# Optimization experiments

Measured on AMD Instinct MI355X. Metric: run time of the kernel, lower is better.

## Reference

```python
import jax, jax.numpy as jnp
import numpy as np
import math

N_LAYERS = 2
N_HEADS = 8
D_MODEL = 512
D_FF = 2048
B = 2
L = 2048
GELU_C = 0.7978845608028654  # sqrt(2/pi)
LN_EPS = 1e-5


def gelu_tanh(x):
    # faithful to the module's custom GELU: 0.5*x*(1+tanh(sqrt(2/pi)*(x+0.044715*x^3)))
    return 0.5 * x * (1.0 + jnp.tanh(GELU_C * (x + 0.044715 * x * x * x)))


def layernorm(x, g, b):
    m = jnp.mean(x, axis=-1, keepdims=True)
    v = jnp.mean((x - m) ** 2, axis=-1, keepdims=True)
    return (x - m) * jax.lax.rsqrt(v + LN_EPS) * g + b


def setup_inputs() -> dict:
    key = jax.random.key(0)
    ks = jax.random.split(key, 24)
    w = lambda k, shape: jax.random.normal(k, shape, dtype=jnp.float32) * 0.02
    inp = {
        "x": jax.random.normal(ks[0], (B, L, D_MODEL), dtype=jnp.float32),
        # tau is exp(tau_learner(...)) in the full model -> positive scalar per batch
        "tau": jax.random.uniform(ks[1], (B, 1), dtype=jnp.float32) + 0.5,
        "delta": jax.random.normal(ks[2], (B, L), dtype=jnp.float32) * 0.1,
        # NStransformer builds an upper-triangular causal mask (True = masked)
        "att_mask": jnp.triu(jnp.ones((L, L), dtype=bool), k=1),
        "Wq": w(ks[3], (N_LAYERS, D_MODEL, D_MODEL)), "bq": jnp.zeros((N_LAYERS, D_MODEL), jnp.float32),
        "Wk": w(ks[4], (N_LAYERS, D_MODEL, D_MODEL)), "bk": jnp.zeros((N_LAYERS, D_MODEL), jnp.float32),
        "Wv": w(ks[5], (N_LAYERS, D_MODEL, D_MODEL)), "bv": jnp.zeros((N_LAYERS, D_MODEL), jnp.float32),
        "Wo": w(ks[6], (N_LAYERS, D_MODEL, D_MODEL)), "bo": jnp.zeros((N_LAYERS, D_MODEL), jnp.float32),
        # conv1/conv2 are kernel_size=1 Conv1d == pointwise linears
        "W1": w(ks[7], (N_LAYERS, D_MODEL, D_FF)), "b1": jnp.zeros((N_LAYERS, D_FF), jnp.float32),
        "W2": w(ks[8], (N_LAYERS, D_FF, D_MODEL)), "b2": jnp.zeros((N_LAYERS, D_MODEL), jnp.float32),
        "ln1_g": jnp.ones((N_LAYERS, D_MODEL), jnp.float32), "ln1_b": jnp.zeros((N_LAYERS, D_MODEL), jnp.float32),
        "ln2_g": jnp.ones((N_LAYERS, D_MODEL), jnp.float32), "ln2_b": jnp.zeros((N_LAYERS, D_MODEL), jnp.float32),
        "lnf_g": jnp.ones((D_MODEL,), jnp.float32), "lnf_b": jnp.zeros((D_MODEL,), jnp.float32),
    }
    return inp


def reference(x, tau, delta, att_mask, Wq, bq, Wk, bk, Wv, bv, Wo, bo,
              W1, b1, W2, b2, ln1_g, ln1_b, ln2_g, ln2_b, lnf_g, lnf_b):
    Bsz, Ls, D = x.shape
    H = N_HEADS
    E = D // H
    scale = 1.0 / math.sqrt(E)
    t = tau[:, None, None, :]    # (B,1) -> (B,1,1,1)
    d = delta[:, None, None, :]  # (B,L) -> (B,1,1,L)
    neg_inf = jnp.float32(-jnp.inf)
    for l in range(N_LAYERS):
        q = (x @ Wq[l] + bq[l]).reshape(Bsz, Ls, H, E)
        k = (x @ Wk[l] + bk[l]).reshape(Bsz, Ls, H, E)
        v = (x @ Wv[l] + bv[l]).reshape(Bsz, Ls, H, E)
        # de-stationary scores: QK^T * tau + delta, then masked softmax
        scores = jnp.einsum('blhe,bshe->bhls', q, k) * t + d  # (B,H,L,S)
        scores = jnp.where(att_mask, neg_inf, scores)
        A = jax.nn.softmax(scale * scores, axis=-1)  # dropout is identity in eval
        V = jnp.einsum('bhls,bshd->blhd', A, v).reshape(Bsz, Ls, D)
        x = (V @ Wo[l] + bo[l]) + x
        xb = layernorm(x, ln1_g[l], ln1_b[l])
        h = gelu_tanh(xb @ W1[l] + b1[l])   # conv1 (k=1)
        o = h @ W2[l] + b2[l]               # conv2 (k=1)
        x = layernorm(o + xb, ln2_g[l], ln2_b[l])
    return layernorm(x, lnf_g, lnf_b)
```

## Files before the change

### kernel.cpp

```cpp
#include <hip/hip_runtime.h>
#include <stdint.h>

#define DM   512
#define DFF  2048
#define NH   8
#define EH   64
#define SEQ  2048
#define NBAT 2
#define NTOK (NBAT*SEQ)
#define LOG2E 1.44269504088896340736f

typedef __attribute__((ext_vector_type(8))) short  s16x8;
typedef __attribute__((ext_vector_type(8))) __bf16 bf16x8;
typedef __attribute__((ext_vector_type(4))) float  f32x4;

__device__ __forceinline__ short f2bf(float f) {
  union { float f; unsigned int i; } c; c.f = f;
  unsigned int x = c.i;
  x += 0x7fffu + ((x >> 16) & 1u);
  return (short)(x >> 16);
}
__device__ __forceinline__ float bf2f(short u) {
  union { unsigned int i; float f; } c;
  c.i = ((unsigned int)(unsigned short)u) << 16;
  return c.f;
}
__device__ __forceinline__ f32x4 mfma16(bf16x8 a, bf16x8 b, f32x4 c) {
  return __builtin_amdgcn_mfma_f32_16x16x32_bf16(a, b, c, 0, 0, 0);
}
__device__ __forceinline__ void gl_lds16(const short* g, short* l) {
  __builtin_amdgcn_global_load_lds(
      (const __attribute__((address_space(1))) unsigned int*)(const void*)g,
      (__attribute__((address_space(3))) unsigned int*)(void*)l, 16, 0, 0);
}

__global__ __launch_bounds__(256) void fill_code_f32(float* __restrict__ out,
                                                     float code)
{
  out[blockIdx.x * 256 + threadIdx.x] = code;
}

__global__ __launch_bounds__(256) void prep_weights(
    const float* __restrict__ Wq, const float* __restrict__ Wk,
    const float* __restrict__ Wv, const float* __restrict__ Wo,
    const float* __restrict__ W1, const float* __restrict__ W2,
    short* __restrict__ Wqkvt, short* __restrict__ Wot,
    short* __restrict__ W1t,   short* __restrict__ W2t)
{
  int gw   = blockIdx.x * 4 + (threadIdx.x >> 6);
  int lane = threadIdx.x & 63;
  int l = gw / 6144;
  int g = gw % 6144;
  const float* src; short* dst; int K, N, gi;
  if (g < 2048) {
    int w = g >> 9; gi = g & 511; K = 512; N = 512;
    src = (w == 0 ? Wq : w == 1 ? Wk : w == 2 ? Wv : Wo) + l * 262144;
    dst = (w < 3) ? (Wqkvt + l * 786432 + w * 262144) : (Wot + l * 262144);
  } else if (g < 4096) {
    gi = g - 2048; K = 512; N = 2048;
    src = W1 + l * 1048576; dst = W1t + l * 1048576;
  } else {
    gi = g - 4096; K = 2048; N = 512;
    src = W2 + l * 1048576; dst = W2t + l * 1048576;
  }
  int nb = N >> 6;
  int n  = (gi % nb) * 64 + lane;
  int k0 = (gi / nb) * 8;
  s16x8 v;
  #pragma unroll
  for (int i = 0; i < 8; i++) v[i] = f2bf(src[(size_t)(k0 + i) * N + n]);
  *(s16x8*)(dst + (size_t)n * K + k0) = v;
}

__global__ __launch_bounds__(256) void cast_kernel(const float* __restrict__ in,
                                                   float* __restrict__ outf,
                                                   short* __restrict__ outb)
{
  int i = blockIdx.x * 256 + threadIdx.x;
  float v = in[i];
  outf[i] = v;
  outb[i] = f2bf(v);
}

template<int TM>
__global__ __launch_bounds__(256) void gemm_bt(
    const short* __restrict__ A, const short* __restrict__ Bt,
    int M, int N, int K, int mode,
    const float* __restrict__ bq, const float* __restrict__ bk,
    const float* __restrict__ bv,
    short* __restrict__ oq, short* __restrict__ okk, short* __restrict__ ov,
    float* of, const float* rf, const short* __restrict__ rb)
{
  __shared__ short As[TM * 32];
  __shared__ short Bs[128 * 32];
  constexpr int MT = TM / 32;
  const int tid  = threadIdx.x;
  const int lane = tid & 63;
  const int wid  = tid >> 6;
  const int lm   = lane & 15, quad = lane >> 4;
  const int nbn  = N >> 7;
  const int m0   = (blockIdx.x / nbn) * TM;
  const int n0   = (blockIdx.x % nbn) << 7;
  const int wm   = (wid & 1) * (TM / 2), wn = (wid >> 1) * 64;

  f32x4 acc[MT][4];
  #pragma unroll
  for (int i = 0; i < MT; i++)
    #pragma unroll
    for (int j = 0; j < 4; j++) acc[i][j] = (f32x4){0.f, 0.f, 0.f, 0.f};

  const short* Abase = A  + (size_t)m0 * K;
  const short* Bbase = Bt + (size_t)n0 * K;

  for (int k0 = 0; k0 < K; k0 += 32) {
    __syncthreads();
    #pragma unroll
    for (int j = 0; j < TM / 64; j++) {
      int c = j * 256 + wid * 64 + lane;
      gl_lds16(Abase + (size_t)(c >> 2) * K + k0 + (c & 3) * 8,
               &As[(j * 256 + wid * 64) * 8]);
    }
    #pragma unroll
    for (int j = 0; j < 2; j++) {
      int c = j * 256 + wid * 64 + lane;
      gl_lds16(Bbase + (size_t)(c >> 2) * K + k0 + (c & 3) * 8,
               &Bs[(j * 256 + wid * 64) * 8]);
    }
    __syncthreads();
    bf16x8 af[MT], bfr[4];
    #pragma unroll
    for (int t = 0; t < MT; t++)
      af[t] = *(const bf16x8*)&As[(wm + t * 16 + lm) * 32 + quad * 8];
    #pragma unroll
    for (int t = 0; t < 4; t++)
      bfr[t] = *(const bf16x8*)&Bs[(wn + t * 16 + lm) * 32 + quad * 8];
    #pragma unroll
    for (int mt = 0; mt < MT; mt++)
      #pragma unroll
      for (int nt = 0; nt < 4; nt++)
        acc[mt][nt] = mfma16(af[mt], bfr[nt], acc[mt][nt]);
  }

  #pragma unroll
  for (int mt = 0; mt < MT; mt++) {
    int row = m0 + wm + mt * 16 + quad * 4;
    #pragma unroll
    for (int nt = 0; nt < 4; nt++) {
      int col = n0 + wn + nt * 16 + lm;
      f32x4 v = acc[mt][nt];
      if (mode == 0) {
        int which = col >> 9; int d = col & 511;
        int hh = d >> 6; int e = d & 63;
        const float* bias = which == 0 ? bq : which == 1 ? bk : bv;
        float bb = bias[d];
        #pragma unroll
        for (int r = 0; r < 4; r++) {
          int tok = row + r; int bI = tok >> 11, li = tok & 2047;
          float val = v[r] + bb;
          if (which == 0)
            oq [(((size_t)bI * NH + hh) * SEQ + li) * EH + e] = f2bf(val);
          else if (which == 1)
            okk[(((size_t)bI * NH + hh) * SEQ + li) * EH + e] = f2bf(val);
          else
            ov [(((size_t)bI * NH + hh) * EH + e) * SEQ + li] = f2bf(val);
        }
      } else if (mode == 1) {
        float bb = bq[col];
        #pragma unroll
        for (int r = 0; r < 4; r++) {
          size_t idx = (size_t)(row + r) * N + col;
          of[idx] = v[r] + bb + rf[idx];
        }
      } else if (mode == 2) {
        float bb = bq[col];
        #pragma unroll
        for (int r = 0; r < 4; r++) {
          float x = v[r] + bb;
          float u = 0.7978845608f * (x + 0.044715f * x * x * x);
          float t = 1.f - 2.f / (1.f + __expf(2.f * u));
          size_t idx = (size_t)(row + r) * N + col;
          oq[idx] = f2bf(0.5f * x * (1.f + t));
        }
      } else {
        float bb = bq[col];
        #pragma unroll
        for (int r = 0; r < 4; r++) {
          size_t idx = (size_t)(row + r) * N + col;
          of[idx] = v[r] + bb + bf2f(rb[idx]);
        }
      }
    }
  }
}

__global__ __launch_bounds__(256) void attn_v7(
    const short* __restrict__ Q, const short* __restrict__ Kg,
    const short* __restrict__ Vt,
    const float* __restrict__ tau, const float* __restrict__ delta,
    short* __restrict__ opart, float* __restrict__ lpart)
{
  __shared__ short Ks[64 * 72];
  __shared__ short Vs[64 * 72];
  __shared__ short Ps[4][16 * 72];
  const int tid  = threadIdx.x;
  const int lane = tid & 63, wid = tid >> 6;
  const int lm = lane & 15, quad = lane >> 4;
  const int t    = blockIdx.x >> 2;
  const int part = blockIdx.x & 3;
  const int qb = 31 - (t & 31);
  const int h  = (t >> 5) & 7;
  const int b  = t >> 8;
  const int q0 = qb * 64;
  const int qw = q0 + wid * 16;
  const size_t bhq = ((size_t)b * NH + h) * SEQ;
  const short* kbase = Kg + bhq * EH;
  const short* vbase = Vt + ((size_t)b * NH + h) * (size_t)(EH * SEQ);

  const int nblk = qb + 1;
  const int kb0 = (nblk * part) >> 2;
  const int kb1 = (nblk * (part + 1)) >> 2;

  bf16x8 qf0 = *(const bf16x8*)(Q + (bhq + qw + lm) * EH + quad * 8);
  bf16x8 qf1 = *(const bf16x8*)(Q + (bhq + qw + lm) * EH + 32 + quad * 8);

  const float st2 = 0.125f * LOG2E * tau[b];
  f32x4 O[4];
  #pragma unroll
  for (int i = 0; i < 4; i++) O[i] = (f32x4){0.f, 0.f, 0.f, 0.f};
  float lr[4] = {0.f, 0.f, 0.f, 0.f};

  const int c0 = tid, c1 = tid + 256;
  const int r0 = c0 >> 3, ch0 = (c0 & 7) * 8;
  const int r1 = c1 >> 3, ch1 = (c1 & 7) * 8;

  for (int kb = kb0; kb < kb1; kb++) {
    const int s0 = kb << 6;
    s16x8 ka = *(const s16x8*)(kbase + (size_t)(s0 + r0) * EH + ch0);
    s16x8 kb_ = *(const s16x8*)(kbase + (size_t)(s0 + r1) * EH + ch1);
    s16x8 va = *(const s16x8*)(vbase + (size_t)r0 * SEQ + s0 + ch0);
    s16x8 vb = *(const s16x8*)(vbase + (size_t)r1 * SEQ + s0 + ch1);
    __syncthreads();
    *(s16x8*)&Ks[r0 * 72 + ch0] = ka;
    *(s16x8*)&Ks[r1 * 72 + ch1] = kb_;
    *(s16x8*)&Vs[r0 * 72 + ch0] = va;
    *(s16x8*)&Vs[r1 * 72 + ch1] = vb;
    __syncthreads();

    f32x4 S[4];
    #pragma unroll
    for (int nt = 0; nt < 4; nt++) {
      S[nt] = (f32x4){0.f, 0.f, 0.f, 0.f};
      S[nt] = mfma16(qf0, *(const bf16x8*)&Ks[(nt*16 + lm) * 72 + quad * 8], S[nt]);
      S[nt] = mfma16(qf1, *(const bf16x8*)&Ks[(nt*16 + lm) * 72 + 32 + quad * 8], S[nt]);
    }
    float dl[4];
    #pragma unroll
    for (int nt = 0; nt < 4; nt++)
      dl[nt] = fmaf(0.125f * LOG2E, delta[(size_t)b * SEQ + s0 + nt * 16 + lm],
                    -8.f);

    const bool diag = (kb == qb);
    #pragma unroll
    for (int r = 0; r < 4; r++) {
      float sc[4];
      #pragma unroll
      for (int nt = 0; nt < 4; nt++) sc[nt] = fmaf(st2, S[nt][r], dl[nt]);
      if (diag) {
        int rowq = qw + quad * 4 + r;
        #pragma unroll
        for (int nt = 0; nt < 4; nt++)
          if (s0 + nt * 16 + lm > rowq) sc[nt] = -__builtin_inff();
      }
      float p0 = exp2f(sc[0]), p1 = exp2f(sc[1]);
      float p2 = exp2f(sc[2]), p3 = exp2f(sc[3]);
      lr[r] += (p0 + p1) + (p2 + p3);
      short* pr = &Ps[wid][(quad * 4 + r) * 72];
      pr[lm]      = f2bf(p0);
      pr[16 + lm] = f2bf(p1);
      pr[32 + lm] = f2bf(p2);
      pr[48 + lm] = f2bf(p3);
    }

    bf16x8 pf0 = *(const bf16x8*)&Ps[wid][lm * 72 + quad * 8];
    bf16x8 pf1 = *(const bf16x8*)&Ps[wid][lm * 72 + 32 + quad * 8];
    #pragma unroll
    for (int et = 0; et < 4; et++) {
      O[et] = mfma16(pf0, *(const bf16x8*)&Vs[(et*16 + lm) * 72 + quad * 8], O[et]);
      O[et] = mfma16(pf1, *(const bf16x8*)&Vs[(et*16 + lm) * 72 + 32 + quad * 8], O[et]);
    }
  }

  #pragma unroll
  for (int r = 0; r < 4; r++) {
    float s = lr[r];
    #pragma unroll
    for (int off = 1; off < 16; off <<= 1) s += __shfl_xor(s, off);
    lr[r] = s;
  }

  const int slot = ((t << 2) | part);
  short* ob = opart + (size_t)slot * 4096;
  float* lb = lpart + (size_t)slot * 64;
  #pragma unroll
  for (int r = 0; r < 4; r++) {
    int qloc = wid * 16 + quad * 4 + r;
    #pragma unroll
    for (int et = 0; et < 4; et++)
      ob[qloc * 64 + et * 16 + lm] = f2bf(O[et][r]);
    if (lm == 0) lb[qloc] = lr[r];
  }
}

__global__ __launch_bounds__(256) void attn_reduce(
    const short* __restrict__ opart, const float* __restrict__ lpart,
    short* __restrict__ Oa)
{
  const int t = blockIdx.x;
  const int qb = 31 - (t & 31);
  const int h  = (t >> 5) & 7;
  const int b  = t >> 8;
  const int q0 = qb * 64;
  #pragma unroll
  for (int i = 0; i < 16; i++) {
    int idx = i * 256 + threadIdx.x;
    int q = idx >> 6, e = idx & 63;
    float l = 0.f, o = 0.f;
    #pragma unroll
    for (int p = 0; p < 4; p++) {
      int slot = t * 4 + p;
      l += lpart[(size_t)slot * 64 + q];
      o += bf2f(opart[(size_t)slot * 4096 + idx]);
    }
    Oa[((size_t)b * SEQ + q0 + q) * DM + h * EH + e] = f2bf(o / l);
  }
}

__global__ __launch_bounds__(256) void ln_kernel(
    const float* in, const float* __restrict__ g, const float* __restrict__ bb,
    float* outf, short* outb)
{
  int row  = blockIdx.x * 4 + (threadIdx.x >> 6);
  int lane = threadIdx.x & 63;
  const float* p = in + (size_t)row * DM;
  float v[8]; float s = 0.f, ss = 0.f;
  #pragma unroll
  for (int i = 0; i < 8; i++) {
    float x = p[lane + i * 64]; v[i] = x; s += x; ss += x * x;
  }
  #pragma unroll
  for (int off = 32; off > 0; off >>= 1) {
    s += __shfl_xor(s, off); ss += __shfl_xor(ss, off);
  }
  float mean = s * (1.f / DM);
  float var  = ss * (1.f / DM) - mean * mean;
  float rstd = rsqrtf(var + 1e-5f);
  #pragma unroll
  for (int i = 0; i < 8; i++) {
    int c = lane + i * 64;
    float y = (v[i] - mean) * rstd * g[c] + bb[c];
    if (outf) outf[(size_t)row * DM + c] = y;
    if (outb) outb[(size_t)row * DM + c] = f2bf(y);
  }
}

extern "C" void kernel_launch(void* const* d_in, const int* in_sizes, int n_in,
                              void* d_out, int out_size, void* d_ws, size_t ws_size,
                              hipStream_t stream)
{
  float* out = (float*)d_out;

  if (ws_size < (size_t)62918656) {
    fill_code_f32<<<2097152 / 256, 256, 0, stream>>>(
        out, 1200.f + (float)(ws_size >> 20));
    return;
  }

  const float* x    = (const float*)d_in[0];
  const float* tau  = (const float*)d_in[1];
  const float* del  = (const float*)d_in[2];
  const float* Wq = (const float*)d_in[4];
  const float* bq = (const float*)d_in[5];
  const float* Wk = (const float*)d_in[6];
  const float* bk = (const float*)d_in[7];
  const float* Wv = (const float*)d_in[8];
  const float* bv = (const float*)d_in[9];
  const float* Wo = (const float*)d_in[10];
  const float* bo = (const float*)d_in[11];
  const float* W1 = (const float*)d_in[12];
  const float* b1 = (const float*)d_in[13];
  const float* W2 = (const float*)d_in[14];
  const float* b2 = (const float*)d_in[15];
  const float* ln1g = (const float*)d_in[16];
  const float* ln1b = (const float*)d_in[17];
  const float* ln2g = (const float*)d_in[18];
  const float* ln2b = (const float*)d_in[19];
  const float* lnfg = (const float*)d_in[20];
  const float* lnfb = (const float*)d_in[21];

  char* ws = (char*)d_ws;
  float* sumf  = (float*)(ws + 0);
  short* x16   = (short*)(ws + 8388608);
  short* xb16  = (short*)(ws + 12582912);
  short* q16   = (short*)(ws + 16777216);
  short* k16   = (short*)(ws + 20971520);
  short* vt16  = (short*)(ws + 25165824);
  short* at16  = (short*)(ws + 29360128);
  short* h16   = (short*)(ws + 33554432);
  short* Wqkvt = (short*)(ws + 50331648);
  short* Wot   = (short*)(ws + 53477376);
  short* W1t   = (short*)(ws + 54525952);
  short* W2t   = (short*)(ws + 58720256);
  short* opart = (short*)(ws + 33554432);
  float* lpart = (float*)(ws + 12582912);

  prep_weights<<<3072, 256, 0, stream>>>(Wq, Wk, Wv, Wo, W1, W2,
                                         Wqkvt, Wot, W1t, W2t);
  cast_kernel<<<NTOK * DM / 256, 256, 0, stream>>>(x, sumf, x16);

  for (int l = 0; l < 2; l++) {
    gemm_bt<64><<<64 * 12, 256, 0, stream>>>(x16, Wqkvt + l * 786432,
        NTOK, 3 * DM, DM, 0,
        bq + l * DM, bk + l * DM, bv + l * DM,
        q16, k16, vt16, nullptr, nullptr, nullptr);
    attn_v7<<<4 * NBAT * NH * (SEQ / 64), 256, 0, stream>>>(
        q16, k16, vt16, tau, del, opart, lpart);
    attn_reduce<<<NBAT * NH * (SEQ / 64), 256, 0, stream>>>(
        opart, lpart, at16);
    gemm_bt<64><<<64 * 4, 256, 0, stream>>>(at16, Wot + l * 262144,
        NTOK, DM, DM, 1,
        bo + l * DM, nullptr, nullptr,
        nullptr, nullptr, nullptr, sumf, sumf, nullptr);
    ln_kernel<<<NTOK / 4, 256, 0, stream>>>(sumf, ln1g + l * DM, ln1b + l * DM,
                                            nullptr, xb16);
    gemm_bt<64><<<64 * 16, 256, 0, stream>>>(xb16, W1t + l * 1048576,
        NTOK, DFF, DM, 2,
        b1 + l * DFF, nullptr, nullptr,
        h16, nullptr, nullptr, nullptr, nullptr, nullptr);
    gemm_bt<64><<<64 * 4, 256, 0, stream>>>(h16, W2t + l * 1048576,
        NTOK, DM, DFF, 3,
        b2 + l * DM, nullptr, nullptr,
        nullptr, nullptr, nullptr, sumf, nullptr, xb16);
    ln_kernel<<<NTOK / 4, 256, 0, stream>>>(sumf, ln2g + l * DM, ln2b + l * DM,
                                            sumf, x16);
  }
  ln_kernel<<<NTOK / 4, 256, 0, stream>>>(sumf, lnfg, lnfb, out, nullptr);
}
```

Measured before the change: 441.0 us.

## Split-K the Wo and W2 GEMMs with bf16 partials and a separate reduce kernel

The N=512 output GEMMs (Wo and W2) previously launched only 256 blocks. They now split K four ways to launch 1024 blocks and write bf16 partial tiles. A new reduction kernel sums the partials and adds the bias and residual into the fp32 stream. This trades extra memory traffic, an extra launch, and bf16 rounding of the partials for better CU occupancy on a device with many CUs.

Result: no change. 437.3 us (-0.9%).

```diff
diff --git a/kernel.cpp b/kernel.cpp
--- a/kernel.cpp
+++ b/kernel.cpp
@@ -82,14 +82,41 @@
   outb[i] = f2bf(v);
 }
 
+__global__ __launch_bounds__(256) void skred(
+    const short* __restrict__ parts, const float* __restrict__ bias,
+    const float* __restrict__ rf, const short* __restrict__ rb,
+    float* __restrict__ of)
+{
+  const int g = blockIdx.x * 256 + threadIdx.x;
+  const size_t base = (size_t)g * 8;
+  float s[8];
+  #pragma unroll
+  for (int j = 0; j < 8; j++) s[j] = bias[(base + j) & 511];
+  #pragma unroll
+  for (int p = 0; p < 4; p++) {
+    s16x8 v = *(const s16x8*)(parts + (size_t)p * 2097152 + base);
+    #pragma unroll
+    for (int j = 0; j < 8; j++) s[j] += bf2f(v[j]);
+  }
+  if (rf) {
+    #pragma unroll
+    for (int j = 0; j < 8; j++) s[j] += rf[base + j];
+  } else {
+    s16x8 v = *(const s16x8*)(rb + base);
+    #pragma unroll
+    for (int j = 0; j < 8; j++) s[j] += bf2f(v[j]);
+  }
+  #pragma unroll
+  for (int j = 0; j < 8; j++) of[base + j] = s[j];
+}
+
 template<int TM>
 __global__ __launch_bounds__(256) void gemm_bt(
     const short* __restrict__ A, const short* __restrict__ Bt,
-    int M, int N, int K, int mode,
+    int M, int N, int K, int KS, int mode,
     const float* __restrict__ bq, const float* __restrict__ bk,
     const float* __restrict__ bv,
-    short* __restrict__ oq, short* __restrict__ okk, short* __restrict__ ov,
-    float* of, const float* rf, const short* __restrict__ rb)
+    short* __restrict__ oq, short* __restrict__ okk, short* __restrict__ ov)
 {
   __shared__ short As[TM * 32];
   __shared__ short Bs[128 * 32];
@@ -99,9 +126,14 @@
   const int wid  = tid >> 6;
   const int lm   = lane & 15, quad = lane >> 4;
   const int nbn  = N >> 7;
-  const int m0   = (blockIdx.x / nbn) * TM;
-  const int n0   = (blockIdx.x % nbn) << 7;
+  const int nb2  = (M / TM) * nbn;
+  const int ks   = blockIdx.x / nb2;
+  const int rem  = blockIdx.x % nb2;
+  const int m0   = (rem / nbn) * TM;
+  const int n0   = (rem % nbn) << 7;
   const int wm   = (wid & 1) * (TM / 2), wn = (wid >> 1) * 64;
+  const int Kc   = K / KS;
+  const int kbeg = ks * Kc;
 
   f32x4 acc[MT][4];
   #pragma unroll
@@ -112,7 +144,7 @@
   const short* Abase = A  + (size_t)m0 * K;
   const short* Bbase = Bt + (size_t)n0 * K;
 
-  for (int k0 = 0; k0 < K; k0 += 32) {
+  for (int k0 = kbeg; k0 < kbeg + Kc; k0 += 32) {
     __syncthreads();
     #pragma unroll
     for (int j = 0; j < TM / 64; j++) {
@@ -164,13 +196,6 @@
           else
             ov [(((size_t)bI * NH + hh) * EH + e) * SEQ + li] = f2bf(val);
         }
-      } else if (mode == 1) {
-        float bb = bq[col];
-        #pragma unroll
-        for (int r = 0; r < 4; r++) {
-          size_t idx = (size_t)(row + r) * N + col;
-          of[idx] = v[r] + bb + rf[idx];
-        }
       } else if (mode == 2) {
         float bb = bq[col];
         #pragma unroll
@@ -182,12 +207,10 @@
           oq[idx] = f2bf(0.5f * x * (1.f + t));
         }
       } else {
-        float bb = bq[col];
+        short* op = oq + (size_t)ks * M * N;
         #pragma unroll
-        for (int r = 0; r < 4; r++) {
-          size_t idx = (size_t)(row + r) * N + col;
-          of[idx] = v[r] + bb + bf2f(rb[idx]);
-        }
+        for (int r = 0; r < 4; r++)
+          op[(size_t)(row + r) * N + col] = f2bf(v[r]);
       }
     }
   }
@@ -410,8 +433,10 @@
   short* Wot   = (short*)(ws + 53477376);
   short* W1t   = (short*)(ws + 54525952);
   short* W2t   = (short*)(ws + 58720256);
-  short* opart = (short*)(ws + 33554432);
-  float* lpart = (float*)(ws + 12582912);
+  short* aopart = (short*)(ws + 33554432);
+  float* alpart = (float*)(ws + 12582912);
+  short* oppart = (short*)(ws + 33554432);
+  short* f2part = (short*)(ws + 16777216);
 
   prep_weights<<<3072, 256, 0, stream>>>(Wq, Wk, Wv, Wo, W1, W2,
                                          Wqkvt, Wot, W1t, W2t);
@@ -419,27 +444,29 @@
 
   for (int l = 0; l < 2; l++) {
     gemm_bt<64><<<64 * 12, 256, 0, stream>>>(x16, Wqkvt + l * 786432,
-        NTOK, 3 * DM, DM, 0,
+        NTOK, 3 * DM, DM, 1, 0,
         bq + l * DM, bk + l * DM, bv + l * DM,
-        q16, k16, vt16, nullptr, nullptr, nullptr);
+        q16, k16, vt16);
     attn_v7<<<4 * NBAT * NH * (SEQ / 64), 256, 0, stream>>>(
-        q16, k16, vt16, tau, del, opart, lpart);
+        q16, k16, vt16, tau, del, aopart, alpart);
     attn_reduce<<<NBAT * NH * (SEQ / 64), 256, 0, stream>>>(
-        opart, lpart, at16);
-    gemm_bt<64><<<64 * 4, 256, 0, stream>>>(at16, Wot + l * 262144,
-        NTOK, DM, DM, 1,
-        bo + l * DM, nullptr, nullptr,
-        nullptr, nullptr, nullptr, sumf, sumf, nullptr);
+        aopart, alpart, at16);
+    gemm_bt<64><<<64 * 4 * 4, 256, 0, stream>>>(at16, Wot + l * 262144,
+        NTOK, DM, DM, 4, 4,
+        nullptr, nullptr, nullptr,
+        oppart, nullptr, nullptr);
+    skred<<<1024, 256, 0, stream>>>(oppart, bo + l * DM, sumf, nullptr, sumf);
     ln_kernel<<<NTOK / 4, 256, 0, stream>>>(sumf, ln1g + l * DM, ln1b + l * DM,
                                             nullptr, xb16);
     gemm_bt<64><<<64 * 16, 256, 0, stream>>>(xb16, W1t + l * 1048576,
-        NTOK, DFF, DM, 2,
+        NTOK, DFF, DM, 1, 2,
         b1 + l * DFF, nullptr, nullptr,
-        h16, nullptr, nullptr, nullptr, nullptr, nullptr);
-    gemm_bt<64><<<64 * 4, 256, 0, stream>>>(h16, W2t + l * 1048576,
-        NTOK, DM, DFF, 3,
-        b2 + l * DM, nullptr, nullptr,
-        nullptr, nullptr, nullptr, sumf, nullptr, xb16);
+        h16, nullptr, nullptr);
+    gemm_bt<64><<<64 * 4 * 4, 256, 0, stream>>>(h16, W2t + l * 1048576,
+        NTOK, DM, DFF, 4, 4,
+        nullptr, nullptr, nullptr,
+        f2part, nullptr, nullptr);
+    skred<<<1024, 256, 0, stream>>>(f2part, b2 + l * DM, nullptr, xb16, sumf);
     ln_kernel<<<NTOK / 4, 256, 0, stream>>>(sumf, ln2g + l * DM, ln2b + l * DM,
                                             sumf, x16);
   }
```
